# Kernel optimization log

Measured on AMD Instinct MI355X. Metric: run time of the kernel, lower is better.

Reference implementation:

```python
import jax, jax.numpy as jnp
import numpy as np

L = 65536
D = 256

def setup_inputs() -> dict:
    key = jax.random.key(0)
    k1, k2, k3 = jax.random.split(key, 3)
    K = jax.random.normal(k1, (L, D), dtype=jnp.float32)
    V = jax.random.normal(k2, (L, D), dtype=jnp.float32)
    q = jax.random.normal(k3, (D,), dtype=jnp.float32)  # nn.Parameter(torch.randn(d_model))
    return {"K": K, "V": V, "q": q, "mode": 0}

def reference(K, V, q, mode):
    # s[i] = <K[i], q>; online-softmax recurrence over the sequence dim.
    s = K @ q  # [L]
    neg_inf = jnp.float32(-jnp.inf)

    def step(carry, inp):
        m_prev, u_prev, w_prev = carry
        s_i, v_i = inp
        m = jnp.maximum(m_prev, s_i)
        e_prev = jnp.exp(m_prev - m)
        e_curr = jnp.exp(s_i - m)
        u = u_prev * e_prev + e_curr
        w = w_prev * e_prev + v_i * e_curr  # [D]
        return (m, u, w), w / u

    init = (neg_inf, jnp.float32(0.0), jnp.zeros((D,), dtype=V.dtype))
    _, out = jax.lax.scan(step, init, (s, V))  # out: [L, D]
    return out
```

## Files before the change

kernel.cpp:

```cpp
#include <hip/hip_runtime.h>
#include <math.h>

#define L_TOTAL 65536
#define D_DIM   256
#define C_ROWS  32
#define N_CHUNK (L_TOTAL / C_ROWS)
#define SUPER   32
#define N_SUPER (N_CHUNK / SUPER)

__global__ __launch_bounds__(256) void kA_aggregate(
    const float* __restrict__ K, const float* __restrict__ V,
    const float* __restrict__ q,
    float* __restrict__ s_g, float* __restrict__ cm,
    float* __restrict__ cu, float* __restrict__ cw)
{
    const int t = threadIdx.x;
    const int c = blockIdx.x;
    const int r0 = c * C_ROWS;
    const int wave = t >> 6, lane = t & 63;

    __shared__ float s_lds[C_ROWS];

    float v[C_ROWS];
    const float* Vp = V + (size_t)r0 * D_DIM + t;
    #pragma unroll
    for (int j = 0; j < C_ROWS; ++j) v[j] = Vp[(size_t)j * D_DIM];

    const float4 q4 = *reinterpret_cast<const float4*>(q + 4 * lane);
    const float* Kp = K + (size_t)(r0 + wave * 8) * D_DIM + 4 * lane;
    float4 kv[8];
    #pragma unroll
    for (int k = 0; k < 8; ++k)
        kv[k] = *reinterpret_cast<const float4*>(Kp + (size_t)k * D_DIM);

    #pragma unroll
    for (int k = 0; k < 8; ++k) {
        float d = kv[k].x * q4.x + kv[k].y * q4.y + kv[k].z * q4.z + kv[k].w * q4.w;
        #pragma unroll
        for (int off = 32; off > 0; off >>= 1) d += __shfl_xor(d, off, 64);
        if (lane == 0) s_lds[wave * 8 + k] = d;
    }
    __syncthreads();

    if (t < C_ROWS) s_g[r0 + t] = s_lds[t];

    float m_c = -INFINITY;
    #pragma unroll
    for (int j = 0; j < C_ROWS; ++j) m_c = fmaxf(m_c, s_lds[j]);

    float u_c = 0.f, w = 0.f;
    #pragma unroll
    for (int j = 0; j < C_ROWS; ++j) {
        const float cf = __expf(s_lds[j] - m_c);
        u_c += cf;
        w = fmaf(cf, v[j], w);
    }

    cw[(size_t)c * D_DIM + t] = w;
    if (t == 0) { cm[c] = m_c; cu[c] = u_c; }
}

__global__ __launch_bounds__(256) void kB_scalar_scan(
    const float* __restrict__ cm, const float* __restrict__ cu,
    float* __restrict__ pm, float* __restrict__ pu)
{
    const int t = threadIdx.x;
    __shared__ float Lm[256], Lu[256];

    float am[8], au[8];
    float M = -INFINITY, U = 0.f;
    #pragma unroll
    for (int j = 0; j < 8; ++j) {
        am[j] = cm[8 * t + j]; au[j] = cu[8 * t + j];
        const float mm = fmaxf(M, am[j]);
        U = U * __expf(M - mm) + au[j] * __expf(am[j] - mm);
        M = mm;
    }
    Lm[t] = M; Lu[t] = U;
    float Mi = M, Ui = U;
    __syncthreads();
    for (int off = 1; off < 256; off <<= 1) {
        float m1 = 0.f, u1 = 0.f;
        const bool act = (t >= off);
        if (act) { m1 = Lm[t - off]; u1 = Lu[t - off]; }
        __syncthreads();
        if (act) {
            const float mm = fmaxf(m1, Mi);
            Ui = u1 * __expf(m1 - mm) + Ui * __expf(Mi - mm);
            Mi = mm;
            Lm[t] = Mi; Lu[t] = Ui;
        }
        __syncthreads();
    }
    float Me = (t == 0) ? -INFINITY : Lm[t - 1];
    float Ue = (t == 0) ? 0.f : Lu[t - 1];
    #pragma unroll
    for (int j = 0; j < 8; ++j) {
        pm[8 * t + j] = Me; pu[8 * t + j] = Ue;
        const float mm = fmaxf(Me, am[j]);
        Ue = Ue * __expf(Me - mm) + au[j] * __expf(am[j] - mm);
        Me = mm;
    }
    if (t == 255) { pm[N_CHUNK] = Me; pu[N_CHUNK] = Ue; }
}

__global__ __launch_bounds__(256) void kC_super_scan(
    const float* __restrict__ cm, const float* __restrict__ cw,
    const float* __restrict__ pm,
    float* __restrict__ pwl, float* __restrict__ T)
{
    const int t = threadIdx.x;
    const int S = blockIdx.x;
    __shared__ float ca[SUPER], cb[SUPER];

    float wv[SUPER];
    const float* cwp = cw + (size_t)S * SUPER * D_DIM + t;
    #pragma unroll
    for (int j = 0; j < SUPER; ++j) wv[j] = cwp[(size_t)j * D_DIM];

    if (t < SUPER) {
        const int c = S * SUPER + t;
        ca[t] = __expf(pm[c] - pm[c + 1]);
        cb[t] = __expf(cm[c] - pm[c + 1]);
    }
    __syncthreads();

    float PW = 0.f;
    float* pwlp = pwl + (size_t)S * SUPER * D_DIM + t;
    #pragma unroll
    for (int j = 0; j < SUPER; ++j) {
        pwlp[(size_t)j * D_DIM] = PW;
        PW = PW * ca[j] + wv[j] * cb[j];
    }
    T[(size_t)S * D_DIM + t] = PW;
}

__global__ __launch_bounds__(256) void kD_top_scan(
    const float* __restrict__ pm, const float* __restrict__ T,
    float* __restrict__ sw)
{
    const int t = threadIdx.x;
    __shared__ float g[N_SUPER];

    float tv[N_SUPER];
    #pragma unroll
    for (int S = 0; S < N_SUPER; ++S) tv[S] = T[(size_t)S * D_DIM + t];

    if (t < N_SUPER)
        g[t] = __expf(pm[t * SUPER] - pm[(t + 1) * SUPER]);
    __syncthreads();

    float SW = 0.f;
    #pragma unroll
    for (int S = 0; S < N_SUPER; ++S) {
        sw[(size_t)S * D_DIM + t] = SW;
        SW = SW * g[S] + tv[S];
    }
}

__global__ __launch_bounds__(256) void kF_output(
    const float* __restrict__ V, const float* __restrict__ s_g,
    const float* __restrict__ pm, const float* __restrict__ pu,
    const float* __restrict__ pwl, const float* __restrict__ sw,
    float* __restrict__ out)
{
    const int t = threadIdx.x;
    const int c = blockIdx.x;
    const int S = c / SUPER;
    const int r0 = c * C_ROWS;
    const int wave = t >> 6, lane = t & 63;

    __shared__ float sa[C_ROWS], se[C_ROWS], sri[C_ROWS];

    float v[C_ROWS];
    const float* Vp = V + (size_t)r0 * D_DIM + t;
    #pragma unroll
    for (int j = 0; j < C_ROWS; ++j) v[j] = Vp[(size_t)j * D_DIM];

    const float seed_pwl = pwl[(size_t)c * D_DIM + t];
    const float seed_sw  = sw[(size_t)S * D_DIM + t];
    const float pmc = pm[c];
    const float pmS = pm[S * SUPER];

    if (wave == 0) {
        const float puc = pu[c];
        float s_val = -INFINITY;
        if (lane < C_ROWS) s_val = s_g[r0 + lane];
        float m = s_val, u = 1.0f;
        #pragma unroll
        for (int off = 1; off < C_ROWS; off <<= 1) {
            const float m1 = __shfl_up(m, off, 32);
            const float u1 = __shfl_up(u, off, 32);
            if ((lane & 31) >= off) {
                const float mm = fmaxf(m1, m);
                u = u1 * __expf(m1 - mm) + u * __expf(m - mm);
                m = mm;
            }
        }
        const float m_row = fmaxf(pmc, m);
        const float u_row = puc * __expf(pmc - m_row) + u * __expf(m - m_row);
        const float m_prev_raw = __shfl_up(m_row, 1, 32);
        const float m_prev = ((lane & 31) == 0) ? pmc : m_prev_raw;
        if (lane < C_ROWS) {
            sa[lane]  = __expf(m_prev - m_row);
            se[lane]  = __expf(s_val - m_row);
            sri[lane] = 1.0f / u_row;
        }
    }
    __syncthreads();

    const float gf = (c == 0) ? 0.f : __expf(pmS - pmc);
    float W = seed_sw * gf + seed_pwl;

    float* Op = out + (size_t)r0 * D_DIM + t;
    #pragma unroll
    for (int j = 0; j < C_ROWS; ++j) {
        W = W * sa[j] + v[j] * se[j];
        Op[(size_t)j * D_DIM] = W * sri[j];
    }
}

extern "C" void kernel_launch(void* const* d_in, const int* in_sizes, int n_in,
                              void* d_out, int out_size, void* d_ws, size_t ws_size,
                              hipStream_t stream) {
    const float* K = (const float*)d_in[0];
    const float* V = (const float*)d_in[1];
    const float* q = (const float*)d_in[2];
    float* out = (float*)d_out;

    float* ws  = (float*)d_ws;
    float* s_g = ws;
    float* cm  = s_g + L_TOTAL;
    float* cu  = cm + N_CHUNK;
    float* pm  = cu + N_CHUNK;
    float* pu  = pm + (N_CHUNK + 16);
    float* cw  = pu + (N_CHUNK + 16);
    float* pwl = cw + (size_t)N_CHUNK * D_DIM;
    float* T   = pwl + (size_t)N_CHUNK * D_DIM;
    float* sw  = T + (size_t)N_SUPER * D_DIM;

    kA_aggregate<<<N_CHUNK, 256, 0, stream>>>(K, V, q, s_g, cm, cu, cw);
    kB_scalar_scan<<<1, 256, 0, stream>>>(cm, cu, pm, pu);
    kC_super_scan<<<N_SUPER, 256, 0, stream>>>(cm, cw, pm, pwl, T);
    kD_top_scan<<<1, 256, 0, stream>>>(pm, T, sw);
    kF_output<<<N_CHUNK, 256, 0, stream>>>(V, s_g, pm, pu, pwl, sw, out);
}
```

Measured before the change: 194.6 us.

## Fuse scan kernels, fold top-level scan into output kernel, add nontemporal K loads/stores

Merges the scalar scan and super-chunk scan into one kernel: every block recomputes the full scalar prefix scan redundantly in LDS, and only block 0 writes pm/pu. The top-level scan over super-chunks is removed, and each output block recomputes its own seed by serially folding up to 63 T rows. This cuts the pipeline from five launches to three. K loads and output stores now use nontemporal hints to reduce cache pollution. The cost is redundant scan work in each block and an extra serial loop of global loads in the output kernel.

```diff
diff --git a/kernel.cpp b/kernel.cpp
--- a/kernel.cpp
+++ b/kernel.cpp
@@ -7,6 +7,8 @@
 #define N_CHUNK (L_TOTAL / C_ROWS)
 #define SUPER   32
 #define N_SUPER (N_CHUNK / SUPER)
+
+typedef float vf4 __attribute__((ext_vector_type(4)));
 
 __global__ __launch_bounds__(256) void kA_aggregate(
     const float* __restrict__ K, const float* __restrict__ V,
@@ -26,12 +28,13 @@
     #pragma unroll
     for (int j = 0; j < C_ROWS; ++j) v[j] = Vp[(size_t)j * D_DIM];
 
-    const float4 q4 = *reinterpret_cast<const float4*>(q + 4 * lane);
+    const vf4 q4 = *reinterpret_cast<const vf4*>(q + 4 * lane);
     const float* Kp = K + (size_t)(r0 + wave * 8) * D_DIM + 4 * lane;
-    float4 kv[8];
+    vf4 kv[8];
     #pragma unroll
     for (int k = 0; k < 8; ++k)
-        kv[k] = *reinterpret_cast<const float4*>(Kp + (size_t)k * D_DIM);
+        kv[k] = __builtin_nontemporal_load(
+                    reinterpret_cast<const vf4*>(Kp + (size_t)k * D_DIM));
 
     #pragma unroll
     for (int k = 0; k < 8; ++k) {
@@ -60,12 +63,18 @@
     if (t == 0) { cm[c] = m_c; cu[c] = u_c; }
 }
 
-__global__ __launch_bounds__(256) void kB_scalar_scan(
+__global__ __launch_bounds__(256) void kCB_scan(
     const float* __restrict__ cm, const float* __restrict__ cu,
-    float* __restrict__ pm, float* __restrict__ pu)
+    const float* __restrict__ cw,
+    float* __restrict__ pm, float* __restrict__ pu,
+    float* __restrict__ gsup,
+    float* __restrict__ pwl, float* __restrict__ T)
 {
     const int t = threadIdx.x;
+    const int S = blockIdx.x;
     __shared__ float Lm[256], Lu[256];
+    __shared__ float pmL[N_CHUNK + 1];
+    __shared__ float ca[SUPER], cb[SUPER];
 
     float am[8], au[8];
     float M = -INFINITY, U = 0.f;
@@ -96,22 +105,17 @@
     float Ue = (t == 0) ? 0.f : Lu[t - 1];
     #pragma unroll
     for (int j = 0; j < 8; ++j) {
-        pm[8 * t + j] = Me; pu[8 * t + j] = Ue;
+        pmL[8 * t + j] = Me;
+        if (S == 0) { pm[8 * t + j] = Me; pu[8 * t + j] = Ue; }
         const float mm = fmaxf(Me, am[j]);
         Ue = Ue * __expf(Me - mm) + au[j] * __expf(am[j] - mm);
         Me = mm;
     }
-    if (t == 255) { pm[N_CHUNK] = Me; pu[N_CHUNK] = Ue; }
-}
-
-__global__ __launch_bounds__(256) void kC_super_scan(
-    const float* __restrict__ cm, const float* __restrict__ cw,
-    const float* __restrict__ pm,
-    float* __restrict__ pwl, float* __restrict__ T)
-{
-    const int t = threadIdx.x;
-    const int S = blockIdx.x;
-    __shared__ float ca[SUPER], cb[SUPER];
+    if (t == 255) {
+        pmL[N_CHUNK] = Me;
+        if (S == 0) { pm[N_CHUNK] = Me; pu[N_CHUNK] = Ue; }
+    }
+    __syncthreads();
 
     float wv[SUPER];
     const float* cwp = cw + (size_t)S * SUPER * D_DIM + t;
@@ -120,9 +124,11 @@
 
     if (t < SUPER) {
         const int c = S * SUPER + t;
-        ca[t] = __expf(pm[c] - pm[c + 1]);
-        cb[t] = __expf(cm[c] - pm[c + 1]);
-    }
+        ca[t] = __expf(pmL[c] - pmL[c + 1]);
+        cb[t] = __expf(cm[c] - pmL[c + 1]);
+    }
+    if (t == 0)
+        gsup[S] = __expf(pmL[S * SUPER] - pmL[S * SUPER + SUPER]);
     __syncthreads();
 
     float PW = 0.f;
@@ -135,33 +141,11 @@
     T[(size_t)S * D_DIM + t] = PW;
 }
 
-__global__ __launch_bounds__(256) void kD_top_scan(
-    const float* __restrict__ pm, const float* __restrict__ T,
-    float* __restrict__ sw)
-{
-    const int t = threadIdx.x;
-    __shared__ float g[N_SUPER];
-
-    float tv[N_SUPER];
-    #pragma unroll
-    for (int S = 0; S < N_SUPER; ++S) tv[S] = T[(size_t)S * D_DIM + t];
-
-    if (t < N_SUPER)
-        g[t] = __expf(pm[t * SUPER] - pm[(t + 1) * SUPER]);
-    __syncthreads();
-
-    float SW = 0.f;
-    #pragma unroll
-    for (int S = 0; S < N_SUPER; ++S) {
-        sw[(size_t)S * D_DIM + t] = SW;
-        SW = SW * g[S] + tv[S];
-    }
-}
-
 __global__ __launch_bounds__(256) void kF_output(
     const float* __restrict__ V, const float* __restrict__ s_g,
     const float* __restrict__ pm, const float* __restrict__ pu,
-    const float* __restrict__ pwl, const float* __restrict__ sw,
+    const float* __restrict__ pwl, const float* __restrict__ T,
+    const float* __restrict__ gsup,
     float* __restrict__ out)
 {
     const int t = threadIdx.x;
@@ -171,6 +155,7 @@
     const int wave = t >> 6, lane = t & 63;
 
     __shared__ float sa[C_ROWS], se[C_ROWS], sri[C_ROWS];
+    __shared__ float gl[N_SUPER];
 
     float v[C_ROWS];
     const float* Vp = V + (size_t)r0 * D_DIM + t;
@@ -178,9 +163,10 @@
     for (int j = 0; j < C_ROWS; ++j) v[j] = Vp[(size_t)j * D_DIM];
 
     const float seed_pwl = pwl[(size_t)c * D_DIM + t];
-    const float seed_sw  = sw[(size_t)S * D_DIM + t];
     const float pmc = pm[c];
     const float pmS = pm[S * SUPER];
+
+    if (t < N_SUPER) gl[t] = gsup[t];
 
     if (wave == 0) {
         const float puc = pu[c];
@@ -209,14 +195,20 @@
     }
     __syncthreads();
 
+    float SW = 0.f;
+    const float* Tp = T + t;
+    #pragma unroll 8
+    for (int Sp = 0; Sp < S; ++Sp)
+        SW = SW * gl[Sp] + Tp[(size_t)Sp * D_DIM];
+
     const float gf = (c == 0) ? 0.f : __expf(pmS - pmc);
-    float W = seed_sw * gf + seed_pwl;
+    float W = SW * gf + seed_pwl;
 
     float* Op = out + (size_t)r0 * D_DIM + t;
     #pragma unroll
     for (int j = 0; j < C_ROWS; ++j) {
         W = W * sa[j] + v[j] * se[j];
-        Op[(size_t)j * D_DIM] = W * sri[j];
+        __builtin_nontemporal_store(W * sri[j], Op + (size_t)j * D_DIM);
     }
 }
 
@@ -228,20 +220,18 @@
     const float* q = (const float*)d_in[2];
     float* out = (float*)d_out;
 
-    float* ws  = (float*)d_ws;
-    float* s_g = ws;
-    float* cm  = s_g + L_TOTAL;
-    float* cu  = cm + N_CHUNK;
-    float* pm  = cu + N_CHUNK;
-    float* pu  = pm + (N_CHUNK + 16);
-    float* cw  = pu + (N_CHUNK + 16);
-    float* pwl = cw + (size_t)N_CHUNK * D_DIM;
-    float* T   = pwl + (size_t)N_CHUNK * D_DIM;
-    float* sw  = T + (size_t)N_SUPER * D_DIM;
+    float* ws   = (float*)d_ws;
+    float* s_g  = ws;
+    float* cm   = s_g + L_TOTAL;
+    float* cu   = cm + N_CHUNK;
+    float* pm   = cu + N_CHUNK;
+    float* pu   = pm + (N_CHUNK + 16);
+    float* gsup = pu + (N_CHUNK + 16);
+    float* cw   = gsup + 128;
+    float* pwl  = cw + (size_t)N_CHUNK * D_DIM;
+    float* T    = pwl + (size_t)N_CHUNK * D_DIM;
 
     kA_aggregate<<<N_CHUNK, 256, 0, stream>>>(K, V, q, s_g, cm, cu, cw);
-    kB_scalar_scan<<<1, 256, 0, stream>>>(cm, cu, pm, pu);
-    kC_super_scan<<<N_SUPER, 256, 0, stream>>>(cm, cw, pm, pwl, T);
-    kD_top_scan<<<1, 256, 0, stream>>>(pm, T, sw);
-    kF_output<<<N_CHUNK, 256, 0, stream>>>(V, s_g, pm, pu, pwl, sw, out);
-}
+    kCB_scan<<<N_SUPER, 256, 0, stream>>>(cm, cu, cw, pm, pu, gsup, pwl, T);
+    kF_output<<<N_CHUNK, 256, 0, stream>>>(V, s_g, pm, pu, pwl, T, gsup, out);
+}
```

Result: faster. 183.1 us (-5.9%).
